# Performance work log

Measured on AMD Instinct MI355X. Metric: run time of the kernel, lower is better.

The kernel has to match this reference:

```python
import jax, jax.numpy as jnp
import numpy as np

B, M = 64, 2048
D_LLM = 4096
D_T, D_P, D_C = 256, 512, 1024
NH_T, NH_P, NH_C = 4, 8, 16
S_T, S_P, S_C = 4, 8, 4
LN_EPS = 1e-5


def setup_inputs() -> dict:
    key = jax.random.key(0)
    ks = iter(jax.random.split(key, 48))
    def n(shape, s=0.02):
        return jax.random.normal(next(ks), shape, jnp.float32) * s
    inp = {
        "hidden_state": jax.random.normal(next(ks), (B, D_LLM), jnp.float32),
        "time_fiber": jax.random.normal(next(ks), (M, D_T), jnp.float32),
        "topic_fiber": jax.random.normal(next(ks), (M, D_P), jnp.float32),
        "ctx_fiber": jax.random.normal(next(ks), (M, D_C), jnp.float32),
        "mem_mask": jnp.zeros((B, M), bool),
        # BundleQueryHeads: Linear(d_LLM -> d_F_*) per bundle (torch weight layout (out,in))
        "Wq_time": n((D_T, D_LLM)), "bq_time": jnp.zeros((D_T,), jnp.float32),
        "Wq_topic": n((D_P, D_LLM)), "bq_topic": jnp.zeros((D_P,), jnp.float32),
        "Wq_ctx": n((D_C, D_LLM)), "bq_ctx": jnp.zeros((D_C,), jnp.float32),
        # nn.MultiheadAttention packed in_proj (3d, d) and out_proj (d, d)
        "Wqkv_time": n((3 * D_T, D_T)), "bqkv_time": jnp.zeros((3 * D_T,), jnp.float32),
        "Wo_time": n((D_T, D_T)), "bo_time": jnp.zeros((D_T,), jnp.float32),
        "Wqkv_topic": n((3 * D_P, D_P)), "bqkv_topic": jnp.zeros((3 * D_P,), jnp.float32),
        "Wo_topic": n((D_P, D_P)), "bo_topic": jnp.zeros((D_P,), jnp.float32),
        "Wqkv_ctx": n((3 * D_C, D_C)), "bqkv_ctx": jnp.zeros((3 * D_C,), jnp.float32),
        "Wo_ctx": n((D_C, D_C)), "bo_ctx": jnp.zeros((D_C,), jnp.float32),
        # per-slot lifts stacked: (slots, d_F, d_LLM) for einsum 'bd,sde->bse'
        "Wlift_time": n((S_T, D_T, D_LLM)), "blift_time": jnp.zeros((S_T, D_LLM), jnp.float32),
        "Wlift_topic": n((S_P, D_P, D_LLM)), "blift_topic": jnp.zeros((S_P, D_LLM), jnp.float32),
        "Wlift_ctx": n((S_C, D_C, D_LLM)), "blift_ctx": jnp.zeros((S_C, D_LLM), jnp.float32),
        "ln_g": jnp.ones((D_LLM,), jnp.float32),
        "ln_b": jnp.zeros((D_LLM,), jnp.float32),
    }
    return inp


def _mha1(q, kv, Wqkv, bqkv, Wo, bo, nh, mask):
    """Single-query-token MHA. q: (B,d); kv: (M,d) shared across batch; mask: (B,M) True=ignore."""
    d = q.shape[-1]
    hd = d // nh
    Wq, Wk, Wv = jnp.split(Wqkv, 3, axis=0)
    bq, bk, bv = jnp.split(bqkv, 3, axis=0)
    qp = (q @ Wq.T + bq).reshape(-1, nh, hd)    # (B,h,hd)
    kp = (kv @ Wk.T + bk).reshape(-1, nh, hd)   # (M,h,hd)
    vp = (kv @ Wv.T + bv).reshape(-1, nh, hd)   # (M,h,hd)
    scale = 1.0 / np.float32(np.sqrt(hd))
    scores = jnp.einsum('bhd,mhd->bhm', qp, kp) * scale  # (B,h,M)
    scores = jnp.where(mask[:, None, :], jnp.float32(-1e9), scores)
    attn = jax.nn.softmax(scores, axis=-1)
    out = jnp.einsum('bhm,mhd->bhd', attn, vp).reshape(-1, d)  # (B,d)
    return out @ Wo.T + bo


def _layernorm(x, g, b):
    mu = jnp.mean(x, axis=-1, keepdims=True)
    var = jnp.mean((x - mu) ** 2, axis=-1, keepdims=True)
    return (x - mu) * jax.lax.rsqrt(var + LN_EPS) * g + b


def reference(hidden_state, time_fiber, topic_fiber, ctx_fiber, mem_mask,
              Wq_time, bq_time, Wq_topic, bq_topic, Wq_ctx, bq_ctx,
              Wqkv_time, bqkv_time, Wo_time, bo_time,
              Wqkv_topic, bqkv_topic, Wo_topic, bo_topic,
              Wqkv_ctx, bqkv_ctx, Wo_ctx, bo_ctx,
              Wlift_time, blift_time, Wlift_topic, blift_topic, Wlift_ctx, blift_ctx,
              ln_g, ln_b):
    # bundle query heads
    q_time = hidden_state @ Wq_time.T + bq_time
    q_topic = hidden_state @ Wq_topic.T + bq_topic
    q_ctx = hidden_state @ Wq_ctx.T + bq_ctx
    # three single-token cross attentions
    o_time = _mha1(q_time, time_fiber, Wqkv_time, bqkv_time, Wo_time, bo_time, NH_T, mem_mask)
    o_topic = _mha1(q_topic, topic_fiber, Wqkv_topic, bqkv_topic, Wo_topic, bo_topic, NH_P, mem_mask)
    o_ctx = _mha1(q_ctx, ctx_fiber, Wqkv_ctx, bqkv_ctx, Wo_ctx, bo_ctx, NH_C, mem_mask)
    # per-slot lifts, batched across slots
    slots_time = jnp.einsum('bd,sde->bse', o_time, Wlift_time) + blift_time[None]
    slots_topic = jnp.einsum('bd,sde->bse', o_topic, Wlift_topic) + blift_topic[None]
    slots_ctx = jnp.einsum('bd,sde->bse', o_ctx, Wlift_ctx) + blift_ctx[None]
    prefix = jnp.concatenate([slots_time, slots_topic, slots_ctx], axis=1)  # (B, L_mem, d_LLM)
    return _layernorm(prefix, ln_g, ln_b)
```

## Files before the change

kernel.cpp:

```cpp
#include <hip/hip_runtime.h>
#include <cstdint>
#include <cstddef>

typedef __attribute__((ext_vector_type(8))) short short8;
typedef __attribute__((ext_vector_type(4))) float floatx4;

__device__ __forceinline__ unsigned short f2bf(float f) {
    unsigned int u = __builtin_bit_cast(unsigned int, f);
    u += 0x7fffu + ((u >> 16) & 1u);
    return (unsigned short)(u >> 16);
}
__device__ __forceinline__ float bflo(unsigned int u) {
    return __builtin_bit_cast(float, u << 16);
}
__device__ __forceinline__ short8 pack8(float4 a, float4 b) {
    short8 r;
    r[0] = (short)f2bf(a.x); r[1] = (short)f2bf(a.y);
    r[2] = (short)f2bf(a.z); r[3] = (short)f2bf(a.w);
    r[4] = (short)f2bf(b.x); r[5] = (short)f2bf(b.y);
    r[6] = (short)f2bf(b.z); r[7] = (short)f2bf(b.w);
    return r;
}

struct SubGemm {
    const float* A; const float* W; const float* bias;
    float* Cf;
    int K, N, Kc, nj, ni, nkz, mode, ldc;
};
struct GemmBatch { SubGemm d[16]; int start[16]; int nd; };

#define MFMA_ALL() { _Pragma("unroll") for (int r_ = 0; r_ < 4; ++r_) { \
    acc[r_][0] = __builtin_amdgcn_mfma_f32_16x16x32_bf16(af[r_], bfr0, acc[r_][0], 0, 0, 0); \
    acc[r_][1] = __builtin_amdgcn_mfma_f32_16x16x32_bf16(af[r_], bfr1, acc[r_][1], 0, 0, 0); } }

#define READ_AF(buf) { _Pragma("unroll") for (int r_ = 0; r_ < 4; ++r_) \
    af[r_] = *(const short8*)&As[buf][aoff[r_]]; }

__global__ __launch_bounds__(256) void gemm_batch(GemmBatch gb)
{
    __shared__ short As[2][64 * 40];

    const int bx = blockIdx.x;
    int di = 0;
#pragma unroll 1
    for (int i = 1; i < gb.nd; ++i) if (bx >= gb.start[i]) di = i;
    const SubGemm g = gb.d[di];
    int local = bx - gb.start[di];
    const int jb = local % g.nj; local /= g.nj;
    const int ib = local % g.ni;
    const int kz = local / g.ni;

    const int tid = threadIdx.x;
    const int w = tid >> 6, lane = tid & 63;
    const int quad = lane >> 4, l16 = lane & 15;
    const int noff = w * 32;

    const int rA = tid >> 2;
    const int sAs = rA * 40 + (((tid & 3) ^ ((rA >> 3) & 3)) << 3);
    const float* pa = g.A + (size_t)(ib * 64 + rA) * g.K + kz * g.Kc + (tid & 3) * 8;

    int aoff[4];
#pragma unroll
    for (int r = 0; r < 4; ++r) {
        int row = r * 16 + l16;
        aoff[r] = row * 40 + ((quad ^ ((row >> 3) & 3)) << 3);
    }

    floatx4 acc[4][2] = {};
    const int steps = g.Kc >> 5;
    short8 af[4], bfr0, bfr1;

    if (g.mode == 1) {
        const float* q0 = g.W + (size_t)(jb * 128 + noff + l16) * g.K + kz * g.Kc + quad * 8;
        const float* q1 = q0 + (size_t)16 * g.K;
        float4 xa0, xa1, ya0, ya1;
        float4 xb0, xb1, xb2, xb3, yb0, yb1, yb2, yb3;
        xa0 = *(const float4*)pa;        xa1 = *(const float4*)(pa + 4);
        xb0 = *(const float4*)q0;        xb1 = *(const float4*)(q0 + 4);
        xb2 = *(const float4*)q1;        xb3 = *(const float4*)(q1 + 4);
        pa += 32; q0 += 32; q1 += 32;
        ya0 = *(const float4*)pa;        ya1 = *(const float4*)(pa + 4);
        yb0 = *(const float4*)q0;        yb1 = *(const float4*)(q0 + 4);
        yb2 = *(const float4*)q1;        yb3 = *(const float4*)(q1 + 4);
        pa += 32; q0 += 32; q1 += 32;
        *(short8*)&As[0][sAs] = pack8(xa0, xa1);
#pragma unroll 1
        for (int s = 0; s < steps; s += 2) {
            __syncthreads();
            READ_AF(0);
            bfr0 = pack8(xb0, xb1); bfr1 = pack8(xb2, xb3);
            MFMA_ALL();
            *(short8*)&As[1][sAs] = pack8(ya0, ya1);
            if (s + 2 < steps) {
                xa0 = *(const float4*)pa; xa1 = *(const float4*)(pa + 4);
                xb0 = *(const float4*)q0; xb1 = *(const float4*)(q0 + 4);
                xb2 = *(const float4*)q1; xb3 = *(const float4*)(q1 + 4);
                pa += 32; q0 += 32; q1 += 32;
            }
            __syncthreads();
            READ_AF(1);
            bfr0 = pack8(yb0, yb1); bfr1 = pack8(yb2, yb3);
            MFMA_ALL();
            if (s + 2 < steps) {
                *(short8*)&As[0][sAs] = pack8(xa0, xa1);
                if (s + 3 < steps) {
                    ya0 = *(const float4*)pa; ya1 = *(const float4*)(pa + 4);
                    yb0 = *(const float4*)q0; yb1 = *(const float4*)(q0 + 4);
                    yb2 = *(const float4*)q1; yb3 = *(const float4*)(q1 + 4);
                    pa += 32; q0 += 32; q1 += 32;
                }
            }
        }
    } else {
        const float* rp[8];
#pragma unroll
        for (int i = 0; i < 8; ++i)
            rp[i] = g.W + ((size_t)(kz * g.Kc) + quad * 8 + i) * g.N
                        + (jb * 128 + noff + l16);
        const size_t bstep = (size_t)32 * g.N;
        float xnb[16], ynb[16];
        float4 xa0, xa1, ya0, ya1;

#define LDB_X() { _Pragma("unroll") for (int i_ = 0; i_ < 8; ++i_) { \
        xnb[i_] = rp[i_][0]; xnb[8 + i_] = rp[i_][16]; rp[i_] += bstep; } }
#define LDB_Y() { _Pragma("unroll") for (int i_ = 0; i_ < 8; ++i_) { \
        ynb[i_] = rp[i_][0]; ynb[8 + i_] = rp[i_][16]; rp[i_] += bstep; } }
#define CVT_X() { _Pragma("unroll") for (int e_ = 0; e_ < 8; ++e_) { \
        bfr0[e_] = (short)f2bf(xnb[e_]); bfr1[e_] = (short)f2bf(xnb[8 + e_]); } }
#define CVT_Y() { _Pragma("unroll") for (int e_ = 0; e_ < 8; ++e_) { \
        bfr0[e_] = (short)f2bf(ynb[e_]); bfr1[e_] = (short)f2bf(ynb[8 + e_]); } }

        xa0 = *(const float4*)pa; xa1 = *(const float4*)(pa + 4); pa += 32;
        LDB_X();
        ya0 = *(const float4*)pa; ya1 = *(const float4*)(pa + 4); pa += 32;
        LDB_Y();
        *(short8*)&As[0][sAs] = pack8(xa0, xa1);
#pragma unroll 1
        for (int s = 0; s < steps; s += 2) {
            __syncthreads();
            READ_AF(0);
            CVT_X();
            MFMA_ALL();
            *(short8*)&As[1][sAs] = pack8(ya0, ya1);
            if (s + 2 < steps) {
                xa0 = *(const float4*)pa; xa1 = *(const float4*)(pa + 4); pa += 32;
                LDB_X();
            }
            __syncthreads();
            READ_AF(1);
            CVT_Y();
            MFMA_ALL();
            if (s + 2 < steps) {
                *(short8*)&As[0][sAs] = pack8(xa0, xa1);
                if (s + 3 < steps) {
                    ya0 = *(const float4*)pa; ya1 = *(const float4*)(pa + 4); pa += 32;
                    LDB_Y();
                }
            }
        }
    }

#pragma unroll
    for (int r = 0; r < 4; ++r)
#pragma unroll
        for (int c = 0; c < 2; ++c) {
            const int col = jb * 128 + noff + c * 16 + l16;
            const float bj = (g.bias != nullptr && kz == 0) ? g.bias[col] : 0.f;
#pragma unroll
            for (int q = 0; q < 4; ++q) {
                const int row = ib * 64 + r * 16 + quad * 4 + q;
                const float v = acc[r][c][q] + bj;
                if (g.nkz > 1) atomicAdd(&g.Cf[(size_t)row * g.ldc + col], v);
                else           g.Cf[(size_t)row * g.ldc + col] = v;
            }
        }
}

struct Sub128 { const float* A; const float* W; const float* bias; unsigned short* C; int K, N, nj; };
struct Batch128 { Sub128 d[4]; int start[4]; int nd; };

__global__ __launch_bounds__(256) void gemm128(Batch128 gb)
{
    __shared__ short As[2][128 * 40];
    __shared__ short Bs[2][128 * 40];

    const int bx = blockIdx.x;
    int di = 0;
#pragma unroll 1
    for (int i = 1; i < gb.nd; ++i) if (bx >= gb.start[i]) di = i;
    const Sub128 g = gb.d[di];
    const int local = bx - gb.start[di];
    const int jb = local % g.nj, ib = local / g.nj;

    const int tid = threadIdx.x;
    const int w = tid >> 6, lane = tid & 63;
    const int quad = lane >> 4, l16 = lane & 15;
    const int wm = (w >> 1) * 64, wn = (w & 1) * 64;

    const int rS = tid >> 1;
    const int gi0 = (tid & 1) * 2;
    const int jsw = (rS >> 3) & 3;
    const int s1 = rS * 40 + ((gi0 ^ jsw) << 3);
    const int s2 = rS * 40 + (((gi0 + 1) ^ jsw) << 3);
    const float* pa = g.A + (size_t)(ib * 128 + rS) * g.K + (tid & 1) * 16;
    const float* pb = g.W + (size_t)(jb * 128 + rS) * g.K + (tid & 1) * 16;

    int aoff[4], boff[4];
#pragma unroll
    for (int r = 0; r < 4; ++r) {
        int rowA = wm + r * 16 + l16;
        aoff[r] = rowA * 40 + ((quad ^ ((rowA >> 3) & 3)) << 3);
        int rowB = wn + r * 16 + l16;
        boff[r] = rowB * 40 + ((quad ^ ((rowB >> 3) & 3)) << 3);
    }

    floatx4 acc[4][4] = {};
    float4 a0 = *(const float4*)pa,       a1 = *(const float4*)(pa + 4);
    float4 a2 = *(const float4*)(pa + 8), a3 = *(const float4*)(pa + 12);
    float4 b0 = *(const float4*)pb,       b1 = *(const float4*)(pb + 4);
    float4 b2 = *(const float4*)(pb + 8), b3 = *(const float4*)(pb + 12);
    *(short8*)&As[0][s1] = pack8(a0, a1);
    *(short8*)&As[0][s2] = pack8(a2, a3);
    *(short8*)&Bs[0][s1] = pack8(b0, b1);
    *(short8*)&Bs[0][s2] = pack8(b2, b3);
    if (g.K > 32) {
        pa += 32; pb += 32;
        a0 = *(const float4*)pa;       a1 = *(const float4*)(pa + 4);
        a2 = *(const float4*)(pa + 8); a3 = *(const float4*)(pa + 12);
        b0 = *(const float4*)pb;       b1 = *(const float4*)(pb + 4);
        b2 = *(const float4*)(pb + 8); b3 = *(const float4*)(pb + 12);
    }
    int cur = 0;
#pragma unroll 1
    for (int k0 = 0; k0 < g.K; k0 += 32) {
        __syncthreads();
        short8 af[4], bf[4];
#pragma unroll
        for (int r = 0; r < 4; ++r) {
            af[r] = *(const short8*)&As[cur][aoff[r]];
            bf[r] = *(const short8*)&Bs[cur][boff[r]];
        }
#pragma unroll
        for (int r = 0; r < 4; ++r)
#pragma unroll
            for (int c = 0; c < 4; ++c)
                acc[r][c] = __builtin_amdgcn_mfma_f32_16x16x32_bf16(af[r], bf[c], acc[r][c], 0, 0, 0);
        if (k0 + 32 < g.K) {
            short* An = As[cur ^ 1]; short* Bn = Bs[cur ^ 1];
            *(short8*)&An[s1] = pack8(a0, a1);
            *(short8*)&An[s2] = pack8(a2, a3);
            *(short8*)&Bn[s1] = pack8(b0, b1);
            *(short8*)&Bn[s2] = pack8(b2, b3);
            if (k0 + 64 < g.K) {
                pa += 32; pb += 32;
                a0 = *(const float4*)pa;       a1 = *(const float4*)(pa + 4);
                a2 = *(const float4*)(pa + 8); a3 = *(const float4*)(pa + 12);
                b0 = *(const float4*)pb;       b1 = *(const float4*)(pb + 4);
                b2 = *(const float4*)(pb + 8); b3 = *(const float4*)(pb + 12);
            }
        }
        cur ^= 1;
    }

#pragma unroll
    for (int r = 0; r < 4; ++r)
#pragma unroll
        for (int c = 0; c < 4; ++c) {
            const int col = jb * 128 + wn + c * 16 + l16;
            const float bj = g.bias[col];
#pragma unroll
            for (int q = 0; q < 4; ++q) {
                const int row = ib * 128 + wm + r * 16 + quad * 4 + q;
                g.C[(size_t)row * g.N + col] = f2bf(acc[r][c][q] + bj);
            }
        }
}

__global__ __launch_bounds__(256) void qk_batch(
    const float* __restrict__ qp_t, const float* __restrict__ qp_p, const float* __restrict__ qp_c,
    const unsigned short* __restrict__ kv_t, const unsigned short* __restrict__ kv_p, const unsigned short* __restrict__ kv_c,
    float* __restrict__ S_t, float* __restrict__ S_p, float* __restrict__ S_c)
{
    __shared__ short As[64 * 72];
    __shared__ short Bs[128 * 72];
    const int hy = blockIdx.y;
    const float* qp; const unsigned short* kv; float* S; int d, h;
    if (hy < 4)       { qp = qp_t; kv = kv_t; S = S_t; d = 256;  h = hy; }
    else if (hy < 12) { qp = qp_p; kv = kv_p; S = S_p; d = 512;  h = hy - 4; }
    else              { qp = qp_c; kv = kv_c; S = S_c; d = 1024; h = hy - 12; }

    const int j0 = blockIdx.x * 128;
    const int tid = threadIdx.x;
    const int w = tid >> 6, lane = tid & 63;
    const int quad = lane >> 4, l16 = lane & 15;
    const int noff = w * 32;
    const int twoD = 2 * d;

    {
        const int b = tid >> 2, kc = (tid & 3) * 16;
        const float* ga = qp + (size_t)b * d + h * 64 + kc;
        float4 a0 = *(const float4*)(ga + 0), a1 = *(const float4*)(ga + 4);
        float4 a2 = *(const float4*)(ga + 8), a3 = *(const float4*)(ga + 12);
        *(short8*)&As[b * 72 + kc + 0] = pack8(a0, a1);
        *(short8*)&As[b * 72 + kc + 8] = pack8(a2, a3);
    }
    {
        const int m = tid >> 1, hf = (tid & 1) * 32;
        const unsigned short* gb = kv + (size_t)(j0 + m) * twoD + h * 64 + hf;
        uint4 b0 = *(const uint4*)(gb + 0),  b1 = *(const uint4*)(gb + 8);
        uint4 b2 = *(const uint4*)(gb + 16), b3 = *(const uint4*)(gb + 24);
        *(uint4*)&Bs[m * 72 + hf + 0]  = b0;
        *(uint4*)&Bs[m * 72 + hf + 8]  = b1;
        *(uint4*)&Bs[m * 72 + hf + 16] = b2;
        *(uint4*)&Bs[m * 72 + hf + 24] = b3;
    }
    __syncthreads();

    floatx4 acc[4][2] = {};
#pragma unroll
    for (int k0 = 0; k0 < 64; k0 += 32) {
        short8 af[4], bfr[2];
#pragma unroll
        for (int r = 0; r < 4; ++r)
            af[r] = *(const short8*)&As[(r * 16 + l16) * 72 + k0 + quad * 8];
#pragma unroll
        for (int c = 0; c < 2; ++c)
            bfr[c] = *(const short8*)&Bs[(noff + c * 16 + l16) * 72 + k0 + quad * 8];
#pragma unroll
        for (int r = 0; r < 4; ++r)
#pragma unroll
            for (int c = 0; c < 2; ++c)
                acc[r][c] = __builtin_amdgcn_mfma_f32_16x16x32_bf16(af[r], bfr[c], acc[r][c], 0, 0, 0);
    }
#pragma unroll
    for (int r = 0; r < 4; ++r)
#pragma unroll
        for (int c = 0; c < 2; ++c) {
            int col = j0 + noff + c * 16 + l16;
#pragma unroll
            for (int q = 0; q < 4; ++q) {
                int row = r * 16 + quad * 4 + q;
                S[((size_t)h * 64 + row) * 2048 + col] = acc[r][c][q] * 0.125f;
            }
        }
}

__global__ __launch_bounds__(256) void softmax_pv_batch(
    const float* __restrict__ S_t, const float* __restrict__ S_p, const float* __restrict__ S_c,
    const unsigned short* __restrict__ kv_t, const unsigned short* __restrict__ kv_p, const unsigned short* __restrict__ kv_c,
    const uint8_t* __restrict__ mask,
    float* __restrict__ o_t, float* __restrict__ o_p, float* __restrict__ o_c)
{
    const int hy = blockIdx.x, b = blockIdx.y;
    const float* S; const unsigned short* kv; float* o; int d, h;
    if (hy < 4)       { S = S_t; kv = kv_t; o = o_t; d = 256;  h = hy; }
    else if (hy < 12) { S = S_p; kv = kv_p; o = o_p; d = 512;  h = hy - 4; }
    else              { S = S_c; kv = kv_c; o = o_c; d = 1024; h = hy - 12; }

    const int tid = threadIdx.x;
    __shared__ __align__(16) float sc[2048];
    __shared__ float red[4];
    __shared__ float part[4][64];
    __shared__ float s_max, s_sum;

    const float* Sr = S + ((size_t)h * 64 + b) * 2048;
    const uint8_t* mr = mask + (size_t)b * 2048;

    float lmax = -1e30f;
    for (int m = tid; m < 2048; m += 256) {
        float s = Sr[m];
        if (mr[m]) s = -1e9f;
        sc[m] = s;
        lmax = fmaxf(lmax, s);
    }
#pragma unroll
    for (int off = 32; off; off >>= 1) lmax = fmaxf(lmax, __shfl_down(lmax, off));
    if ((tid & 63) == 0) red[tid >> 6] = lmax;
    __syncthreads();
    if (tid == 0) s_max = fmaxf(fmaxf(red[0], red[1]), fmaxf(red[2], red[3]));
    __syncthreads();
    const float mx = s_max;

    float lsum = 0.f;
    for (int m = tid; m < 2048; m += 256) {
        float e = __expf(sc[m] - mx);
        sc[m] = e;
        lsum += e;
    }
#pragma unroll
    for (int off = 32; off; off >>= 1) lsum += __shfl_down(lsum, off);
    if ((tid & 63) == 0) red[tid >> 6] = lsum;
    __syncthreads();
    if (tid == 0) s_sum = red[0] + red[1] + red[2] + red[3];
    __syncthreads();

    const int lane = tid & 63, w = tid >> 6;
    const int twoD = 2 * d;
    const unsigned short* vcol = kv + d + h * 64 + lane;
    float acc = 0.f;
    const int m0 = w * 512;
#pragma unroll 1
    for (int m = m0; m < m0 + 512; m += 8) {
#pragma unroll
        for (int j = 0; j < 8; ++j)
            acc += sc[m + j] * bflo((unsigned int)vcol[(size_t)(m + j) * twoD]);
    }
    part[w][lane] = acc;
    __syncthreads();
    if (tid < 64) {
        float r = (part[0][tid] + part[1][tid] + part[2][tid] + part[3][tid]) / s_sum;
        o[(size_t)b * d + h * 64 + tid] = r;
    }
}

__global__ __launch_bounds__(256) void ln_kernel(
    float* __restrict__ x, const float* __restrict__ g, const float* __restrict__ bb,
    const float* __restrict__ blt, const float* __restrict__ blp, const float* __restrict__ blc)
{
    const int row = blockIdx.x;
    const int l = row & 15;
    const float* lb = (l < 4)  ? (blt + (size_t)l * 4096)
                    : (l < 12) ? (blp + (size_t)(l - 4) * 4096)
                               : (blc + (size_t)(l - 12) * 4096);
    float* xr = x + (size_t)row * 4096;
    const int tid = threadIdx.x;
    float v[16];
    float sum = 0.f, sumsq = 0.f;
#pragma unroll
    for (int i = 0; i < 16; ++i) {
        int e = tid + i * 256;
        v[i] = xr[e] + lb[e];
        sum += v[i];
        sumsq += v[i] * v[i];
    }
    __shared__ float rs[4], rq[4];
#pragma unroll
    for (int off = 32; off; off >>= 1) {
        sum += __shfl_down(sum, off);
        sumsq += __shfl_down(sumsq, off);
    }
    if ((tid & 63) == 0) { rs[tid >> 6] = sum; rq[tid >> 6] = sumsq; }
    __syncthreads();
    const float ts = rs[0] + rs[1] + rs[2] + rs[3];
    const float tq = rq[0] + rq[1] + rq[2] + rq[3];
    const float mu = ts * (1.f / 4096.f);
    const float var = tq * (1.f / 4096.f) - mu * mu;
    const float r = rsqrtf(var + 1e-5f);
#pragma unroll
    for (int i = 0; i < 16; ++i) {
        int e = tid + i * 256;
        xr[e] = (v[i] - mu) * r * g[e] + bb[e];
    }
}

static void addg(GemmBatch& G, int& tot,
                 const float* A, const float* W, const float* bias, float* Cf,
                 int K, int N, int Kc, int nj, int ni, int nkz, int mode, int ldc)
{
    SubGemm& s = G.d[G.nd];
    s.A = A; s.W = W; s.bias = bias; s.Cf = Cf;
    s.K = K; s.N = N; s.Kc = Kc; s.nj = nj; s.ni = ni; s.nkz = nkz;
    s.mode = mode; s.ldc = ldc;
    G.start[G.nd] = tot;
    tot += nj * ni * nkz;
    G.nd++;
}
static void add128(Batch128& G, int& tot,
                   const float* A, const float* W, const float* bias, unsigned short* C,
                   int K, int N, int nj, int ni)
{
    Sub128& s = G.d[G.nd];
    s.A = A; s.W = W; s.bias = bias; s.C = C; s.K = K; s.N = N; s.nj = nj;
    G.start[G.nd] = tot;
    tot += nj * ni;
    G.nd++;
}

extern "C" void kernel_launch(void* const* d_in, const int* in_sizes, int n_in,
                              void* d_out, int out_size, void* d_ws, size_t ws_size,
                              hipStream_t stream)
{
    const float*   hs     = (const float*)d_in[0];
    const float*   fib_t  = (const float*)d_in[1];
    const float*   fib_p  = (const float*)d_in[2];
    const float*   fib_c  = (const float*)d_in[3];
    const uint8_t* mask   = (const uint8_t*)d_in[4];
    const float* Wq_t   = (const float*)d_in[5];  const float* bq_t   = (const float*)d_in[6];
    const float* Wq_p   = (const float*)d_in[7];  const float* bq_p   = (const float*)d_in[8];
    const float* Wq_c   = (const float*)d_in[9];  const float* bq_c   = (const float*)d_in[10];
    const float* Wqkv_t = (const float*)d_in[11]; const float* bqkv_t = (const float*)d_in[12];
    const float* Wo_t   = (const float*)d_in[13]; const float* bo_t   = (const float*)d_in[14];
    const float* Wqkv_p = (const float*)d_in[15]; const float* bqkv_p = (const float*)d_in[16];
    const float* Wo_p   = (const float*)d_in[17]; const float* bo_p   = (const float*)d_in[18];
    const float* Wqkv_c = (const float*)d_in[19]; const float* bqkv_c = (const float*)d_in[20];
    const float* Wo_c   = (const float*)d_in[21]; const float* bo_c   = (const float*)d_in[22];
    const float* Wl_t   = (const float*)d_in[23]; const float* bl_t   = (const float*)d_in[24];
    const float* Wl_p   = (const float*)d_in[25]; const float* bl_p   = (const float*)d_in[26];
    const float* Wl_c   = (const float*)d_in[27]; const float* bl_c   = (const float*)d_in[28];
    const float* ln_g   = (const float*)d_in[29]; const float* ln_b   = (const float*)d_in[30];

    char* wsb = (char*)d_ws;
    float* q_t  = (float*)wsb; wsb += 64 * 256 * 4;
    float* q_p  = (float*)wsb; wsb += 64 * 512 * 4;
    float* q_c  = (float*)wsb; wsb += 64 * 1024 * 4;
    float* qp_t = (float*)wsb; wsb += 64 * 256 * 4;
    float* qp_p = (float*)wsb; wsb += 64 * 512 * 4;
    float* qp_c = (float*)wsb; wsb += 64 * 1024 * 4;
    float* po_t = (float*)wsb; wsb += 64 * 256 * 4;
    float* po_p = (float*)wsb; wsb += 64 * 512 * 4;
    float* po_c = (float*)wsb; wsb += 64 * 1024 * 4;
    size_t zbytes = (size_t)(wsb - (char*)d_ws);
    float* o_t  = (float*)wsb; wsb += 64 * 256 * 4;
    float* o_p  = (float*)wsb; wsb += 64 * 512 * 4;
    float* o_c  = (float*)wsb; wsb += 64 * 1024 * 4;
    unsigned short* kv_t = (unsigned short*)wsb; wsb += 2048 * 512 * 2;
    unsigned short* kv_p = (unsigned short*)wsb; wsb += 2048 * 1024 * 2;
    unsigned short* kv_c = (unsigned short*)wsb; wsb += 2048 * 2048 * 2;
    float* S_t = (float*)wsb; wsb += (size_t)4  * 64 * 2048 * 4;
    float* S_p = (float*)wsb; wsb += (size_t)8  * 64 * 2048 * 4;
    float* S_c = (float*)wsb; wsb += (size_t)16 * 64 * 2048 * 4;
    float* out = (float*)d_out;

    const dim3 blk(256);
    hipMemsetAsync(d_ws, 0, zbytes, stream);
    hipMemsetAsync(d_out, 0, (size_t)out_size, stream);

    {
        GemmBatch G{}; int tot = 0; G.nd = 0;
        addg(G, tot, hs, Wq_c, bq_c, q_c, 4096, 1024, 256, 8, 1, 16, 1, 1024);
        addg(G, tot, hs, Wq_p, bq_p, q_p, 4096, 512,  256, 4, 1, 16, 1, 512);
        addg(G, tot, hs, Wq_t, bq_t, q_t, 4096, 256,  256, 2, 1, 16, 1, 256);
        gemm_batch<<<dim3(tot), blk, 0, stream>>>(G);
    }

    {
        Batch128 G{}; int tot = 0; G.nd = 0;
        add128(G, tot, fib_c, Wqkv_c + 1024 * 1024, bqkv_c + 1024, kv_c, 1024, 2048, 16, 16);
        add128(G, tot, fib_p, Wqkv_p + 512 * 512,   bqkv_p + 512,  kv_p, 512,  1024, 8,  16);
        add128(G, tot, fib_t, Wqkv_t + 256 * 256,   bqkv_t + 256,  kv_t, 256,  512,  4,  16);
        gemm128<<<dim3(tot), blk, 0, stream>>>(G);
    }

    {
        GemmBatch G{}; int tot = 0; G.nd = 0;
        addg(G, tot, q_c, Wqkv_c, bqkv_c, qp_c, 1024, 1024, 128, 8, 1, 8, 1, 1024);
        addg(G, tot, q_p, Wqkv_p, bqkv_p, qp_p, 512,  512,  64,  4, 1, 8, 1, 512);
        addg(G, tot, q_t, Wqkv_t, bqkv_t, qp_t, 256,  256,  64,  2, 1, 4, 1, 256);
        gemm_batch<<<dim3(tot), blk, 0, stream>>>(G);
    }

    qk_batch<<<dim3(16, 28), blk, 0, stream>>>(qp_t, qp_p, qp_c, kv_t, kv_p, kv_c, S_t, S_p, S_c);
    softmax_pv_batch<<<dim3(28, 64), blk, 0, stream>>>(S_t, S_p, S_c, kv_t, kv_p, kv_c, mask, o_t, o_p, o_c);

    {
        GemmBatch G{}; int tot = 0; G.nd = 0;
        addg(G, tot, o_c, Wo_c, bo_c, po_c, 1024, 1024, 128, 8, 1, 8, 1, 1024);
        addg(G, tot, o_p, Wo_p, bo_p, po_p, 512,  512,  64,  4, 1, 8, 1, 512);
        addg(G, tot, o_t, Wo_t, bo_t, po_t, 256,  256,  64,  2, 1, 4, 1, 256);
        gemm_batch<<<dim3(tot), blk, 0, stream>>>(G);
    }

    {
        GemmBatch G{}; int tot = 0; G.nd = 0;
        for (int z = 0; z < 4; ++z)
            addg(G, tot, po_c, Wl_c + (size_t)z * 1024 * 4096, nullptr,
                 out + (size_t)(12 + z) * 4096, 1024, 4096, 256, 32, 1, 4, 2, 16 * 4096);
        for (int z = 0; z < 8; ++z)
            addg(G, tot, po_p, Wl_p + (size_t)z * 512 * 4096, nullptr,
                 out + (size_t)(4 + z) * 4096, 512, 4096, 256, 32, 1, 2, 2, 16 * 4096);
        for (int z = 0; z < 4; ++z)
            addg(G, tot, po_t, Wl_t + (size_t)z * 256 * 4096, nullptr,
                 out + (size_t)z * 4096, 256, 4096, 256, 32, 1, 1, 2, 16 * 4096);
        gemm_batch<<<dim3(tot), blk, 0, stream>>>(G);
    }

    ln_kernel<<<dim3(1024), blk, 0, stream>>>(out, ln_g, ln_b, bl_t, bl_p, bl_c);
}
```

Baseline: 407.1 us.

## Replace block GEMMs with single-wave GEMMs and split softmax from MFMA PV

Swaps the 256-thread shared-memory batched GEMM for a 64-thread wave GEMM that loads A directly into registers with no LDS or barriers. It retiles with smaller N chunks and different split-K factors. The fused softmax+PV kernel becomes a softmax kernel that writes normalized probabilities back, followed by an MFMA-based PV kernel with split-K atomics. The lift GEMM now writes directly without split-K and adds bias in the epilogue, which removes the output memset and the bias addition in layernorm. This trades LDS reuse of A across waves for more parallel small blocks and redundant A loads, and adds an extra pass over the score matrix.

```diff
diff --git a/kernel.cpp b/kernel.cpp
--- a/kernel.cpp
+++ b/kernel.cpp
@@ -9,9 +9,6 @@
     unsigned int u = __builtin_bit_cast(unsigned int, f);
     u += 0x7fffu + ((u >> 16) & 1u);
     return (unsigned short)(u >> 16);
-}
-__device__ __forceinline__ float bflo(unsigned int u) {
-    return __builtin_bit_cast(float, u << 16);
 }
 __device__ __forceinline__ short8 pack8(float4 a, float4 b) {
     short8 r;
@@ -22,141 +19,91 @@
     return r;
 }
 
-struct SubGemm {
-    const float* A; const float* W; const float* bias;
-    float* Cf;
-    int K, N, Kc, nj, ni, nkz, mode, ldc;
+struct WaveG {
+    const float* A; const float* W; const float* bias; float* C;
+    int K, Kc, ldw, ldc, nj, nkz, mode;
 };
-struct GemmBatch { SubGemm d[16]; int start[16]; int nd; };
+struct WaveBatch { WaveG d[16]; int start[16]; int nd; };
 
 #define MFMA_ALL() { _Pragma("unroll") for (int r_ = 0; r_ < 4; ++r_) { \
     acc[r_][0] = __builtin_amdgcn_mfma_f32_16x16x32_bf16(af[r_], bfr0, acc[r_][0], 0, 0, 0); \
     acc[r_][1] = __builtin_amdgcn_mfma_f32_16x16x32_bf16(af[r_], bfr1, acc[r_][1], 0, 0, 0); } }
 
-#define READ_AF(buf) { _Pragma("unroll") for (int r_ = 0; r_ < 4; ++r_) \
-    af[r_] = *(const short8*)&As[buf][aoff[r_]]; }
-
-__global__ __launch_bounds__(256) void gemm_batch(GemmBatch gb)
-{
-    __shared__ short As[2][64 * 40];
-
+#define LOADA(dst) { _Pragma("unroll") for (int r_ = 0; r_ < 4; ++r_) { \
+    dst[r_][0] = *(const float4*)pa[r_]; dst[r_][1] = *(const float4*)(pa[r_] + 4); \
+    pa[r_] += 32; } }
+
+#define PACKA(src) { _Pragma("unroll") for (int r_ = 0; r_ < 4; ++r_) \
+    af[r_] = pack8(src[r_][0], src[r_][1]); }
+
+__global__ __launch_bounds__(64) void wave_gemm(WaveBatch wb)
+{
     const int bx = blockIdx.x;
     int di = 0;
 #pragma unroll 1
-    for (int i = 1; i < gb.nd; ++i) if (bx >= gb.start[i]) di = i;
-    const SubGemm g = gb.d[di];
-    int local = bx - gb.start[di];
-    const int jb = local % g.nj; local /= g.nj;
-    const int ib = local % g.ni;
-    const int kz = local / g.ni;
-
-    const int tid = threadIdx.x;
-    const int w = tid >> 6, lane = tid & 63;
+    for (int i = 1; i < wb.nd; ++i) if (bx >= wb.start[i]) di = i;
+    const WaveG g = wb.d[di];
+    int local = bx - wb.start[di];
+    const int j = local % g.nj;
+    const int kz = local / g.nj;
+
+    const int lane = threadIdx.x;
     const int quad = lane >> 4, l16 = lane & 15;
-    const int noff = w * 32;
-
-    const int rA = tid >> 2;
-    const int sAs = rA * 40 + (((tid & 3) ^ ((rA >> 3) & 3)) << 3);
-    const float* pa = g.A + (size_t)(ib * 64 + rA) * g.K + kz * g.Kc + (tid & 3) * 8;
-
-    int aoff[4];
-#pragma unroll
-    for (int r = 0; r < 4; ++r) {
-        int row = r * 16 + l16;
-        aoff[r] = row * 40 + ((quad ^ ((row >> 3) & 3)) << 3);
-    }
+
+    const float* pa[4];
+#pragma unroll
+    for (int r = 0; r < 4; ++r)
+        pa[r] = g.A + (size_t)(r * 16 + l16) * g.K + kz * g.Kc + quad * 8;
 
     floatx4 acc[4][2] = {};
     const int steps = g.Kc >> 5;
     short8 af[4], bfr0, bfr1;
 
-    if (g.mode == 1) {
-        const float* q0 = g.W + (size_t)(jb * 128 + noff + l16) * g.K + kz * g.Kc + quad * 8;
-        const float* q1 = q0 + (size_t)16 * g.K;
-        float4 xa0, xa1, ya0, ya1;
-        float4 xb0, xb1, xb2, xb3, yb0, yb1, yb2, yb3;
-        xa0 = *(const float4*)pa;        xa1 = *(const float4*)(pa + 4);
-        xb0 = *(const float4*)q0;        xb1 = *(const float4*)(q0 + 4);
-        xb2 = *(const float4*)q1;        xb3 = *(const float4*)(q1 + 4);
-        pa += 32; q0 += 32; q1 += 32;
-        ya0 = *(const float4*)pa;        ya1 = *(const float4*)(pa + 4);
-        yb0 = *(const float4*)q0;        yb1 = *(const float4*)(q0 + 4);
-        yb2 = *(const float4*)q1;        yb3 = *(const float4*)(q1 + 4);
-        pa += 32; q0 += 32; q1 += 32;
-        *(short8*)&As[0][sAs] = pack8(xa0, xa1);
+    if (g.mode == 0) {
+        const float* pb0 = g.W + (size_t)(j * 32 + l16) * g.K + kz * g.Kc + quad * 8;
+        const float* pb1 = pb0 + (size_t)16 * g.K;
+        float4 xa[4][2], ya[4][2];
+        float4 xb[2][2], yb[2][2];
+#define LOADB_NT(dst) { dst[0][0] = *(const float4*)pb0; dst[0][1] = *(const float4*)(pb0 + 4); \
+        dst[1][0] = *(const float4*)pb1; dst[1][1] = *(const float4*)(pb1 + 4); \
+        pb0 += 32; pb1 += 32; }
+        LOADA(xa); LOADB_NT(xb);
+        LOADA(ya); LOADB_NT(yb);
 #pragma unroll 1
         for (int s = 0; s < steps; s += 2) {
-            __syncthreads();
-            READ_AF(0);
-            bfr0 = pack8(xb0, xb1); bfr1 = pack8(xb2, xb3);
+            PACKA(xa);
+            bfr0 = pack8(xb[0][0], xb[0][1]); bfr1 = pack8(xb[1][0], xb[1][1]);
             MFMA_ALL();
-            *(short8*)&As[1][sAs] = pack8(ya0, ya1);
-            if (s + 2 < steps) {
-                xa0 = *(const float4*)pa; xa1 = *(const float4*)(pa + 4);
-                xb0 = *(const float4*)q0; xb1 = *(const float4*)(q0 + 4);
-                xb2 = *(const float4*)q1; xb3 = *(const float4*)(q1 + 4);
-                pa += 32; q0 += 32; q1 += 32;
-            }
-            __syncthreads();
-            READ_AF(1);
-            bfr0 = pack8(yb0, yb1); bfr1 = pack8(yb2, yb3);
+            if (s + 2 < steps) { LOADA(xa); LOADB_NT(xb); }
+            PACKA(ya);
+            bfr0 = pack8(yb[0][0], yb[0][1]); bfr1 = pack8(yb[1][0], yb[1][1]);
             MFMA_ALL();
-            if (s + 2 < steps) {
-                *(short8*)&As[0][sAs] = pack8(xa0, xa1);
-                if (s + 3 < steps) {
-                    ya0 = *(const float4*)pa; ya1 = *(const float4*)(pa + 4);
-                    yb0 = *(const float4*)q0; yb1 = *(const float4*)(q0 + 4);
-                    yb2 = *(const float4*)q1; yb3 = *(const float4*)(q1 + 4);
-                    pa += 32; q0 += 32; q1 += 32;
-                }
-            }
+            if (s + 3 < steps) { LOADA(ya); LOADB_NT(yb); }
         }
     } else {
-        const float* rp[8];
+        const float* pw[8];
 #pragma unroll
         for (int i = 0; i < 8; ++i)
-            rp[i] = g.W + ((size_t)(kz * g.Kc) + quad * 8 + i) * g.N
-                        + (jb * 128 + noff + l16);
-        const size_t bstep = (size_t)32 * g.N;
-        float xnb[16], ynb[16];
-        float4 xa0, xa1, ya0, ya1;
-
-#define LDB_X() { _Pragma("unroll") for (int i_ = 0; i_ < 8; ++i_) { \
-        xnb[i_] = rp[i_][0]; xnb[8 + i_] = rp[i_][16]; rp[i_] += bstep; } }
-#define LDB_Y() { _Pragma("unroll") for (int i_ = 0; i_ < 8; ++i_) { \
-        ynb[i_] = rp[i_][0]; ynb[8 + i_] = rp[i_][16]; rp[i_] += bstep; } }
-#define CVT_X() { _Pragma("unroll") for (int e_ = 0; e_ < 8; ++e_) { \
-        bfr0[e_] = (short)f2bf(xnb[e_]); bfr1[e_] = (short)f2bf(xnb[8 + e_]); } }
-#define CVT_Y() { _Pragma("unroll") for (int e_ = 0; e_ < 8; ++e_) { \
-        bfr0[e_] = (short)f2bf(ynb[e_]); bfr1[e_] = (short)f2bf(ynb[8 + e_]); } }
-
-        xa0 = *(const float4*)pa; xa1 = *(const float4*)(pa + 4); pa += 32;
-        LDB_X();
-        ya0 = *(const float4*)pa; ya1 = *(const float4*)(pa + 4); pa += 32;
-        LDB_Y();
-        *(short8*)&As[0][sAs] = pack8(xa0, xa1);
+            pw[i] = g.W + ((size_t)(kz * g.Kc) + quad * 8 + i) * g.ldw + j * 32 + l16;
+        const size_t ldw32 = (size_t)32 * g.ldw;
+        float4 xa[4][2], ya[4][2];
+        float xb[16], yb[16];
+#define LOADB_NN(dst) { _Pragma("unroll") for (int i_ = 0; i_ < 8; ++i_) { \
+        dst[i_] = pw[i_][0]; dst[8 + i_] = pw[i_][16]; pw[i_] += ldw32; } }
+#define CVTB(src) { _Pragma("unroll") for (int e_ = 0; e_ < 8; ++e_) { \
+        bfr0[e_] = (short)f2bf(src[e_]); bfr1[e_] = (short)f2bf(src[8 + e_]); } }
+        LOADA(xa); LOADB_NN(xb);
+        LOADA(ya); LOADB_NN(yb);
 #pragma unroll 1
         for (int s = 0; s < steps; s += 2) {
-            __syncthreads();
-            READ_AF(0);
-            CVT_X();
+            PACKA(xa);
+            CVTB(xb);
             MFMA_ALL();
-            *(short8*)&As[1][sAs] = pack8(ya0, ya1);
-            if (s + 2 < steps) {
-                xa0 = *(const float4*)pa; xa1 = *(const float4*)(pa + 4); pa += 32;
-                LDB_X();
-            }
-            __syncthreads();
-            READ_AF(1);
-            CVT_Y();
+            if (s + 2 < steps) { LOADA(xa); LOADB_NN(xb); }
+            PACKA(ya);
+            CVTB(yb);
             MFMA_ALL();
-            if (s + 2 < steps) {
-                *(short8*)&As[0][sAs] = pack8(xa0, xa1);
-                if (s + 3 < steps) {
-                    ya0 = *(const float4*)pa; ya1 = *(const float4*)(pa + 4); pa += 32;
-                    LDB_Y();
-                }
-            }
+            if (s + 3 < steps) { LOADA(ya); LOADB_NN(yb); }
         }
     }
 
@@ -164,14 +111,14 @@
     for (int r = 0; r < 4; ++r)
 #pragma unroll
         for (int c = 0; c < 2; ++c) {
-            const int col = jb * 128 + noff + c * 16 + l16;
-            const float bj = (g.bias != nullptr && kz == 0) ? g.bias[col] : 0.f;
+            const int col = j * 32 + c * 16 + l16;
+            const float bj = (kz == 0) ? g.bias[col] : 0.f;
 #pragma unroll
             for (int q = 0; q < 4; ++q) {
-                const int row = ib * 64 + r * 16 + quad * 4 + q;
+                const int row = r * 16 + quad * 4 + q;
                 const float v = acc[r][c][q] + bj;
-                if (g.nkz > 1) atomicAdd(&g.Cf[(size_t)row * g.ldc + col], v);
-                else           g.Cf[(size_t)row * g.ldc + col] = v;
+                if (g.nkz > 1) atomicAdd(&g.C[(size_t)row * g.ldc + col], v);
+                else           g.C[(size_t)row * g.ldc + col] = v;
             }
         }
 }
@@ -345,25 +292,22 @@
         }
 }
 
-__global__ __launch_bounds__(256) void softmax_pv_batch(
-    const float* __restrict__ S_t, const float* __restrict__ S_p, const float* __restrict__ S_c,
-    const unsigned short* __restrict__ kv_t, const unsigned short* __restrict__ kv_p, const unsigned short* __restrict__ kv_c,
-    const uint8_t* __restrict__ mask,
-    float* __restrict__ o_t, float* __restrict__ o_p, float* __restrict__ o_c)
+__global__ __launch_bounds__(256) void softmax_p(
+    float* __restrict__ S_t, float* __restrict__ S_p, float* __restrict__ S_c,
+    const uint8_t* __restrict__ mask)
 {
     const int hy = blockIdx.x, b = blockIdx.y;
-    const float* S; const unsigned short* kv; float* o; int d, h;
-    if (hy < 4)       { S = S_t; kv = kv_t; o = o_t; d = 256;  h = hy; }
-    else if (hy < 12) { S = S_p; kv = kv_p; o = o_p; d = 512;  h = hy - 4; }
-    else              { S = S_c; kv = kv_c; o = o_c; d = 1024; h = hy - 12; }
+    float* S; int h;
+    if (hy < 4)       { S = S_t; h = hy; }
+    else if (hy < 12) { S = S_p; h = hy - 4; }
+    else              { S = S_c; h = hy - 12; }
 
     const int tid = threadIdx.x;
     __shared__ __align__(16) float sc[2048];
     __shared__ float red[4];
-    __shared__ float part[4][64];
     __shared__ float s_max, s_sum;
 
-    const float* Sr = S + ((size_t)h * 64 + b) * 2048;
+    float* Sr = S + ((size_t)h * 64 + b) * 2048;
     const uint8_t* mr = mask + (size_t)b * 2048;
 
     float lmax = -1e30f;
@@ -393,43 +337,77 @@
     __syncthreads();
     if (tid == 0) s_sum = red[0] + red[1] + red[2] + red[3];
     __syncthreads();
-
-    const int lane = tid & 63, w = tid >> 6;
+    const float inv = 1.f / s_sum;
+
+    for (int m = tid; m < 2048; m += 256) Sr[m] = sc[m] * inv;
+}
+
+__global__ __launch_bounds__(64) void pv_batch(
+    const float* __restrict__ P_t, const float* __restrict__ P_p, const float* __restrict__ P_c,
+    const unsigned short* __restrict__ kv_t, const unsigned short* __restrict__ kv_p, const unsigned short* __restrict__ kv_c,
+    float* __restrict__ o_t, float* __restrict__ o_p, float* __restrict__ o_c)
+{
+    const int hy = blockIdx.x, kz = blockIdx.y;
+    const float* P; const unsigned short* kv; float* o; int d, h;
+    if (hy < 4)       { P = P_t; kv = kv_t; o = o_t; d = 256;  h = hy; }
+    else if (hy < 12) { P = P_p; kv = kv_p; o = o_p; d = 512;  h = hy - 4; }
+    else              { P = P_c; kv = kv_c; o = o_c; d = 1024; h = hy - 12; }
+
+    const int lane = threadIdx.x;
+    const int quad = lane >> 4, l16 = lane & 15;
     const int twoD = 2 * d;
-    const unsigned short* vcol = kv + d + h * 64 + lane;
-    float acc = 0.f;
-    const int m0 = w * 512;
+
+    const float* pa[4];
+#pragma unroll
+    for (int r = 0; r < 4; ++r)
+        pa[r] = P + ((size_t)h * 64 + r * 16 + l16) * 2048 + kz * 256 + quad * 8;
+    const unsigned short* pb = kv + (size_t)(kz * 256 + quad * 8) * twoD + d + h * 64 + l16;
+
+    floatx4 acc[4][4] = {};
 #pragma unroll 1
-    for (int m = m0; m < m0 + 512; m += 8) {
-#pragma unroll
-        for (int j = 0; j < 8; ++j)
-            acc += sc[m + j] * bflo((unsigned int)vcol[(size_t)(m + j) * twoD]);
-    }
-    part[w][lane] = acc;
-    __syncthreads();
-    if (tid < 64) {
-        float r = (part[0][tid] + part[1][tid] + part[2][tid] + part[3][tid]) / s_sum;
-        o[(size_t)b * d + h * 64 + tid] = r;
-    }
+    for (int s = 0; s < 8; ++s) {
+        short8 af[4];
+#pragma unroll
+        for (int r = 0; r < 4; ++r) {
+            float4 a0 = *(const float4*)pa[r], a1 = *(const float4*)(pa[r] + 4);
+            af[r] = pack8(a0, a1);
+            pa[r] += 32;
+        }
+        short8 bf[4];
+#pragma unroll
+        for (int c = 0; c < 4; ++c)
+#pragma unroll
+            for (int i = 0; i < 8; ++i)
+                bf[c][i] = (short)pb[(size_t)i * twoD + c * 16];
+        pb += (size_t)32 * twoD;
+#pragma unroll
+        for (int r = 0; r < 4; ++r)
+#pragma unroll
+            for (int c = 0; c < 4; ++c)
+                acc[r][c] = __builtin_amdgcn_mfma_f32_16x16x32_bf16(af[r], bf[c], acc[r][c], 0, 0, 0);
+    }
+#pragma unroll
+    for (int r = 0; r < 4; ++r)
+#pragma unroll
+        for (int c = 0; c < 4; ++c)
+#pragma unroll
+            for (int q = 0; q < 4; ++q) {
+                const int row = r * 16 + quad * 4 + q;
+                atomicAdd(&o[(size_t)row * d + h * 64 + c * 16 + l16], acc[r][c][q]);
+            }
 }
 
 __global__ __launch_bounds__(256) void ln_kernel(
-    float* __restrict__ x, const float* __restrict__ g, const float* __restrict__ bb,
-    const float* __restrict__ blt, const float* __restrict__ blp, const float* __restrict__ blc)
+    float* __restrict__ x, const float* __restrict__ g, const float* __restrict__ bb)
 {
     const int row = blockIdx.x;
-    const int l = row & 15;
-    const float* lb = (l < 4)  ? (blt + (size_t)l * 4096)
-                    : (l < 12) ? (blp + (size_t)(l - 4) * 4096)
-                               : (blc + (size_t)(l - 12) * 4096);
     float* xr = x + (size_t)row * 4096;
     const int tid = threadIdx.x;
     float v[16];
     float sum = 0.f, sumsq = 0.f;
 #pragma unroll
     for (int i = 0; i < 16; ++i) {
-        int e = tid + i * 256;
-        v[i] = xr[e] + lb[e];
+        v[i] = xr[tid + i * 256];
         sum += v[i];
         sumsq += v[i] * v[i];
     }
@@ -453,16 +431,15 @@
     }
 }
 
-static void addg(GemmBatch& G, int& tot,
-                 const float* A, const float* W, const float* bias, float* Cf,
-                 int K, int N, int Kc, int nj, int ni, int nkz, int mode, int ldc)
-{
-    SubGemm& s = G.d[G.nd];
-    s.A = A; s.W = W; s.bias = bias; s.Cf = Cf;
-    s.K = K; s.N = N; s.Kc = Kc; s.nj = nj; s.ni = ni; s.nkz = nkz;
-    s.mode = mode; s.ldc = ldc;
+static void addw(WaveBatch& G, int& tot,
+                 const float* A, const float* W, const float* bias, float* C,
+                 int K, int Kc, int ldw, int ldc, int nj, int nkz, int mode)
+{
+    WaveG& s = G.d[G.nd];
+    s.A = A; s.W = W; s.bias = bias; s.C = C;
+    s.K = K; s.Kc = Kc; s.ldw = ldw; s.ldc = ldc; s.nj = nj; s.nkz = nkz; s.mode = mode;
     G.start[G.nd] = tot;
-    tot += nj * ni * nkz;
+    tot += nj * nkz;
     G.nd++;
 }
 static void add128(Batch128& G, int& tot,
@@ -509,10 +486,10 @@
     float* po_t = (float*)wsb; wsb += 64 * 256 * 4;
     float* po_p = (float*)wsb; wsb += 64 * 512 * 4;
     float* po_c = (float*)wsb; wsb += 64 * 1024 * 4;
-    size_t zbytes = (size_t)(wsb - (char*)d_ws);
     float* o_t  = (float*)wsb; wsb += 64 * 256 * 4;
     float* o_p  = (float*)wsb; wsb += 64 * 512 * 4;
     float* o_c  = (float*)wsb; wsb += 64 * 1024 * 4;
+    size_t zbytes = (size_t)(wsb - (char*)d_ws);
     unsigned short* kv_t = (unsigned short*)wsb; wsb += 2048 * 512 * 2;
     unsigned short* kv_p = (unsigned short*)wsb; wsb += 2048 * 1024 * 2;
     unsigned short* kv_c = (unsigned short*)wsb; wsb += 2048 * 2048 * 2;
@@ -521,16 +498,14 @@
     float* S_c = (float*)wsb; wsb += (size_t)16 * 64 * 2048 * 4;
     float* out = (float*)d_out;
 
-    const dim3 blk(256);
     hipMemsetAsync(d_ws, 0, zbytes, stream);
-    hipMemsetAsync(d_out, 0, (size_t)out_size, stream);
-
-    {
-        GemmBatch G{}; int tot = 0; G.nd = 0;
-        addg(G, tot, hs, Wq_c, bq_c, q_c, 4096, 1024, 256, 8, 1, 16, 1, 1024);
-        addg(G, tot, hs, Wq_p, bq_p, q_p, 4096, 512,  256, 4, 1, 16, 1, 512);
-        addg(G, tot, hs, Wq_t, bq_t, q_t, 4096, 256,  256, 2, 1, 16, 1, 256);
-        gemm_batch<<<dim3(tot), blk, 0, stream>>>(G);
+
+    {
+        WaveBatch G{}; int tot = 0; G.nd = 0;
+        addw(G, tot, hs, Wq_c, bq_c, q_c, 4096, 256, 0, 1024, 32, 16, 0);
+        addw(G, tot, hs, Wq_p, bq_p, q_p, 4096, 256, 0, 512,  16, 16, 0);
+        addw(G, tot, hs, Wq_t, bq_t, q_t, 4096, 256, 0, 256,  8,  16, 0);
+        wave_gemm<<<dim3(tot), dim3(64), 0, stream>>>(G);
     }
 
     {
@@ -538,41 +513,42 @@
         add128(G, tot, fib_c, Wqkv_c + 1024 * 1024, bqkv_c + 1024, kv_c, 1024, 2048, 16, 16);
         add128(G, tot, fib_p, Wqkv_p + 512 * 512,   bqkv_p + 512,  kv_p, 512,  1024, 8,  16);
         add128(G, tot, fib_t, Wqkv_t + 256 * 256,   bqkv_t + 256,  kv_t, 256,  512,  4,  16);
-        gemm128<<<dim3(tot), blk, 0, stream>>>(G);
-    }
-
-    {
-        GemmBatch G{}; int tot = 0; G.nd = 0;
-        addg(G, tot, q_c, Wqkv_c, bqkv_c, qp_c, 1024, 1024, 128, 8, 1, 8, 1, 1024);
-        addg(G, tot, q_p, Wqkv_p, bqkv_p, qp_p, 512,  512,  64,  4, 1, 8, 1, 512);
-        addg(G, tot, q_t, Wqkv_t, bqkv_t, qp_t, 256,  256,  64,  2, 1, 4, 1, 256);
-        gemm_batch<<<dim3(tot), blk, 0, stream>>>(G);
-    }
-
-    qk_batch<<<dim3(16, 28), blk, 0, stream>>>(qp_t, qp_p, qp_c, kv_t, kv_p, kv_c, S_t, S_p, S_c);
-    softmax_pv_batch<<<dim3(28, 64), blk, 0, stream>>>(S_t, S_p, S_c, kv_t, kv_p, kv_c, mask, o_t, o_p, o_c);
-
-    {
-        GemmBatch G{}; int tot = 0; G.nd = 0;
-        addg(G, tot, o_c, Wo_c, bo_c, po_c, 1024, 1024, 128, 8, 1, 8, 1, 1024);
-        addg(G, tot, o_p, Wo_p, bo_p, po_p, 512,  512,  64,  4, 1, 8, 1, 512);
-        addg(G, tot, o_t, Wo_t, bo_t, po_t, 256,  256,  64,  2, 1, 4, 1, 256);
-        gemm_batch<<<dim3(tot), blk, 0, stream>>>(G);
-    }
-
-    {
-        GemmBatch G{}; int tot = 0; G.nd = 0;
+        gemm128<<<dim3(tot), dim3(256), 0, stream>>>(G);
+    }
+
+    {
+        WaveBatch G{}; int tot = 0; G.nd = 0;
+        addw(G, tot, q_c, Wqkv_c, bqkv_c, qp_c, 1024, 256, 0, 1024, 32, 4, 0);
+        addw(G, tot, q_p, Wqkv_p, bqkv_p, qp_p, 512,  256, 0, 512,  16, 2, 0);
+        addw(G, tot, q_t, Wqkv_t, bqkv_t, qp_t, 256,  256, 0, 256,  8,  1, 0);
+        wave_gemm<<<dim3(tot), dim3(64), 0, stream>>>(G);
+    }
+
+    qk_batch<<<dim3(16, 28), dim3(256), 0, stream>>>(qp_t, qp_p, qp_c, kv_t, kv_p, kv_c, S_t, S_p, S_c);
+    softmax_p<<<dim3(28, 64), dim3(256), 0, stream>>>(S_t, S_p, S_c, mask);
+    pv_batch<<<dim3(28, 8), dim3(64), 0, stream>>>(S_t, S_p, S_c, kv_t, kv_p, kv_c, o_t, o_p, o_c);
+
+    {
+        WaveBatch G{}; int tot = 0; G.nd = 0;
+        addw(G, tot, o_c, Wo_c, bo_c, po_c, 1024, 256, 0, 1024, 32, 4, 0);
+        addw(G, tot, o_p, Wo_p, bo_p, po_p, 512,  256, 0, 512,  16, 2, 0);
+        addw(G, tot, o_t, Wo_t, bo_t, po_t, 256,  256, 0, 256,  8,  1, 0);
+        wave_gemm<<<dim3(tot), dim3(64), 0, stream>>>(G);
+    }
+
+    {
+        WaveBatch G{}; int tot = 0; G.nd = 0;
         for (int z = 0; z < 4; ++z)
-            addg(G, tot, po_c, Wl_c + (size_t)z * 1024 * 4096, nullptr,
-                 out + (size_t)(12 + z) * 4096, 1024, 4096, 256, 32, 1, 4, 2, 16 * 4096);
+            addw(G, tot, po_c, Wl_c + (size_t)z * 1024 * 4096, bl_c + z * 4096,
+                 out + (size_t)(12 + z) * 4096, 1024, 1024, 4096, 16 * 4096, 128, 1, 1);
         for (int z = 0; z < 8; ++z)
-            addg(G, tot, po_p, Wl_p + (size_t)z * 512 * 4096, nullptr,
-                 out + (size_t)(4 + z) * 4096, 512, 4096, 256, 32, 1, 2, 2, 16 * 4096);
+            addw(G, tot, po_p, Wl_p + (size_t)z * 512 * 4096, bl_p + z * 4096,
+                 out + (size_t)(4 + z) * 4096, 512, 512, 4096, 16 * 4096, 128, 1, 1);
         for (int z = 0; z < 4; ++z)
-            addg(G, tot, po_t, Wl_t + (size_t)z * 256 * 4096, nullptr,
-                 out + (size_t)z * 4096, 256, 4096, 256, 32, 1, 1, 2, 16 * 4096);
-        gemm_batch<<<dim3(tot), blk, 0, stream>>>(G);
-    }
-
-    ln_kernel<<<dim3(1024), blk, 0, stream>>>(out, ln_g, ln_b, bl_t, bl_p, bl_c);
-}
+            addw(G, tot, po_t, Wl_t + (size_t)z * 256 * 4096, bl_t + z * 4096,
+                 out + (size_t)z * 4096, 256, 256, 4096, 16 * 4096, 128, 1, 1);
+        wave_gemm<<<dim3(tot), dim3(64), 0, stream>>>(G);
+    }
+
+    ln_kernel<<<dim3(1024), dim3(256), 0, stream>>>(out, ln_g, ln_b);
+}
```

Result: faster. 388.0 us (-4.7%).
